# Kernel optimization log

Hardware: AMD Instinct MI355X
Metric: run time of the kernel (lower is better)

The kernel has to match this reference:

```python
import jax, jax.numpy as jnp
import numpy as np
from jax import lax

N, T, L, H, C, D, Q = 8, 8, 257, 16, 64, 1024, 256


def _ln(x, w, b, eps=1e-5):
    m = x.mean(-1, keepdims=True)
    v = ((x - m) ** 2).mean(-1, keepdims=True)
    return (x - m) * lax.rsqrt(v + eps) * w + b


def _quick_gelu(x):
    return x * jax.nn.sigmoid(1.702 * x)


def _adaptor(x, ln_w, ln_b, w1, w2):
    # LayerNorm -> Linear(d, d//8, bias=False) -> Linear(d//8, d, bias=False)
    h = _ln(x, ln_w, ln_b)
    return (h @ w1.T) @ w2.T


def setup_inputs() -> dict:
    key = jax.random.key(0)
    ks = jax.random.split(key, 16)
    f32 = jnp.float32
    inp = {
        'attrs_k': jax.random.normal(ks[0], (N, T, L, H, C), f32),
        'attrs_v': jax.random.normal(ks[1], (N, T, L, H, C), f32),
        's': jax.random.normal(ks[2], (N, Q, D), f32),
        'te': jax.random.normal(ks[3], (T, D), f32),
        'patch_mask': jax.random.normal(ks[4], (1, 1, Q, L - 1, 1), f32) * 0.1,
        'ln1_w': jnp.ones((D,), f32), 'ln1_b': jnp.zeros((D,), f32),
        'in_proj_w': jax.random.normal(ks[5], (3 * D, D), f32) * 0.02,
        'in_proj_b': jnp.zeros((3 * D,), f32),
        'out_proj_w': jax.random.normal(ks[6], (D, D), f32) * 0.02,
        'out_proj_b': jnp.zeros((D,), f32),
        'ln2_w': jnp.ones((D,), f32), 'ln2_b': jnp.zeros((D,), f32),
        'c_fc_w': jax.random.normal(ks[7], (4 * D, D), f32) * 0.02,
        'c_fc_b': jnp.zeros((4 * D,), f32),
        'c_proj_w': jax.random.normal(ks[8], (D, 4 * D), f32) * 0.02,
        'c_proj_b': jnp.zeros((D,), f32),
        'syno_ln_w': jnp.ones((D,), f32), 'syno_ln_b': jnp.zeros((D,), f32),
        'syno_l1_w': jax.random.normal(ks[9], (D // 8, D), f32) * 0.001,
        'syno_l2_w': jax.random.normal(ks[10], (D, D // 8), f32) * 0.001,
        'te_ln_w': jnp.ones((D,), f32), 'te_ln_b': jnp.zeros((D,), f32),
        'te_l1_w': jax.random.normal(ks[11], (D // 8, D), f32) * 0.001,
        'te_l2_w': jax.random.normal(ks[12], (D, D // 8), f32) * 0.001,
        'tconv_w': jax.random.normal(ks[13], (D, 1, 3), f32) * 0.001,
        'tconv_b': jnp.zeros((D,), f32),
    }
    return inp


def reference(attrs_k, attrs_v, s, te, patch_mask,
              ln1_w, ln1_b, in_proj_w, in_proj_b, out_proj_w, out_proj_b,
              ln2_w, ln2_b, c_fc_w, c_fc_b, c_proj_w, c_proj_b,
              syno_ln_w, syno_ln_b, syno_l1_w, syno_l2_w,
              te_ln_w, te_ln_b, te_l1_w, te_l2_w, tconv_w, tconv_b):
    n, q, d = s.shape
    t = te.shape[0]
    h = H
    c = d // h

    # adaptors (forward())
    _te = _adaptor(te, te_ln_w, te_ln_b, te_l1_w, te_l2_w) + te
    _s = s + _adaptor(s, syno_ln_w, syno_ln_b, syno_l1_w, syno_l2_w)
    x = _ln(_s, ln1_w, ln1_b)

    # qkv projections
    qkv = x @ in_proj_w.T + in_proj_b
    s_q, _, _ = jnp.split(qkv, 3, axis=-1)
    s_q = s_q.reshape(n, q, h, c)
    te_qkv = _te @ in_proj_w.T + in_proj_b
    _, te_k, te_v = jnp.split(te_qkv, 3, axis=-1)
    te_k = te_k.reshape(t, 1, h, c)  # broadcasts over batch and k dims
    te_v = te_v.reshape(t, 1, h, c)

    _k = attrs_k[:, :, 1:]  # drop CLS -> [n,t,K,h,c]
    _v = attrs_v[:, :, 1:]

    scale = 1.0 / jnp.sqrt(jnp.asarray(c, s_q.dtype))
    s_aff = jnp.einsum('nqhc,ntkhc->ntqkh', s_q * scale, _k + te_k) + patch_mask
    s_aff = jax.nn.softmax(s_aff, axis=-2)  # over k
    s_mix = jnp.einsum('ntqkh,ntkhc->ntqhc', s_aff, _v + te_v)

    # residual depthwise temporal conv over t: [n,t,q,h,c] -> [n*q, d, t]
    xm = s_mix.transpose(0, 2, 3, 4, 1).reshape(n * q, d, t)
    y = lax.conv_general_dilated(xm, tconv_w, window_strides=(1,), padding=[(1, 1)],
                                 feature_group_count=d,
                                 dimension_numbers=('NCH', 'OIH', 'NCH'))
    xm = (y + tconv_b[None, :, None]) + xm
    s_mix = xm.reshape(n, q, h, c, t).transpose(0, 4, 1, 2, 3)  # [n,t,q,h,c]

    s_mix = s_mix.mean(axis=1)  # mean over time -> [n,q,h,c]
    s_out = s_mix.reshape(n, q, d) @ out_proj_w.T + out_proj_b

    # residual + MLP (CLIP-style QuickGELU)
    s1 = s + s_out
    hmid = _quick_gelu(_ln(s1, ln2_w, ln2_b) @ c_fc_w.T + c_fc_b)
    s1 = s1 + (hmid @ c_proj_w.T + c_proj_b)
    return s1
```

## Files before the change

kernel.cpp:

```cpp
#include <hip/hip_runtime.h>

#define NN 8
#define TT 8
#define LL 257
#define HH 16
#define CC 64
#define DD 1024
#define QQ 256
#define NQ (NN*QQ)

typedef __attribute__((ext_vector_type(4))) float f32x4;
typedef __attribute__((ext_vector_type(4))) unsigned int u32x4;
typedef __attribute__((ext_vector_type(2))) unsigned int u32x2;

static __device__ __forceinline__ float4 ld4(const float* p) { return *(const float4*)p; }

static __device__ __forceinline__ void mfma16(f32x4& d, u32x4 a, u32x4 b) {
  asm("v_mfma_f32_16x16x32_bf16 %0, %1, %2, %0" : "+v"(d) : "v"(a), "v"(b));
}

static __device__ __forceinline__ unsigned int f2bf(float x) {
  unsigned int u = __float_as_uint(x);
  return (u + 0x7fffu + ((u >> 16) & 1u)) >> 16;
}
static __device__ __forceinline__ unsigned int pk2(float lo, float hi) {
  return f2bf(lo) | (f2bf(hi) << 16);
}
static __device__ __forceinline__ unsigned int cvtpk(float lo, float hi) {
  unsigned int r;
  asm("v_cvt_pk_bf16_f32 %0, %1, %2" : "=v"(r) : "v"(lo), "v"(hi));
  return r;
}
static __device__ __forceinline__ float bf2f(unsigned int u) {
  return __uint_as_float(u << 16);
}

typedef __attribute__((address_space(3))) unsigned char lds_t;
typedef const __attribute__((address_space(1))) unsigned char glb_t;
static __device__ __forceinline__ void gld16(const void* g, void* l) {
  __builtin_amdgcn_global_load_lds((glb_t*)g, (lds_t*)l, 16, 0, 0);
}

__global__ __launch_bounds__(256) void cvt_bf16_kernel(const float* __restrict__ in,
    unsigned short* __restrict__ out, int n4) {
  const int i = blockIdx.x * 256 + threadIdx.x;
  if (i < n4) {
    const float4 v = ld4(in + (size_t)i * 4);
    u32x2 p; p.x = pk2(v.x, v.y); p.y = pk2(v.z, v.w);
    *(u32x2*)(out + (size_t)i * 4) = p;
  }
}

__global__ __launch_bounds__(256) void ln_bf_kernel(const float* __restrict__ in,
    const float* __restrict__ w, const float* __restrict__ b, unsigned short* __restrict__ out) {
  __shared__ float red[16];
  const int tid = threadIdx.x;
  const size_t row = blockIdx.x;
  const float4 v = ((const float4*)(in + row * DD))[tid];
  float s  = v.x + v.y + v.z + v.w;
  float ss = v.x*v.x + v.y*v.y + v.z*v.z + v.w*v.w;
  #pragma unroll
  for (int off = 32; off; off >>= 1) { s += __shfl_xor(s, off); ss += __shfl_xor(ss, off); }
  if ((tid & 63) == 0) { red[tid >> 6] = s; red[8 + (tid >> 6)] = ss; }
  __syncthreads();
  s  = red[0] + red[1] + red[2] + red[3];
  ss = red[8] + red[9] + red[10] + red[11];
  const float mean = s * (1.f / DD);
  const float var  = ss * (1.f / DD) - mean * mean;
  const float inv  = rsqrtf(var + 1e-5f);
  const float4 wv = ((const float4*)w)[tid];
  const float4 bv = ((const float4*)b)[tid];
  float o0 = (v.x - mean) * inv * wv.x + bv.x;
  float o1 = (v.y - mean) * inv * wv.y + bv.y;
  float o2 = (v.z - mean) * inv * wv.z + bv.z;
  float o3 = (v.w - mean) * inv * wv.w + bv.w;
  u32x2 p; p.x = pk2(o0, o1); p.y = pk2(o2, o3);
  *(u32x2*)(out + row * DD + tid * 4) = p;
}

__global__ __launch_bounds__(256) void te_mid_kernel(
    const unsigned short* __restrict__ telnb, const float* __restrict__ l1,
    float* __restrict__ midf) {
  const int j = blockIdx.x * 4 + (threadIdx.x >> 6);
  const int l = threadIdx.x & 63;
  const float* lr = l1 + (size_t)j * DD + l * 16;
  float wv[16];
  #pragma unroll
  for (int q = 0; q < 4; ++q) {
    const float4 f = ld4(lr + q * 4);
    wv[q*4] = f.x; wv[q*4+1] = f.y; wv[q*4+2] = f.z; wv[q*4+3] = f.w;
  }
  float acc[8];
  #pragma unroll
  for (int t = 0; t < 8; ++t) {
    const unsigned short* hp = telnb + (size_t)t * DD + l * 16;
    const u32x4 h0 = *(const u32x4*)hp;
    const u32x4 h1 = *(const u32x4*)(hp + 8);
    float a = 0.f;
    #pragma unroll
    for (int e = 0; e < 4; ++e) {
      a += bf2f(h0[e] & 0xffffu) * wv[e*2]   + bf2f(h0[e] >> 16) * wv[e*2+1];
      a += bf2f(h1[e] & 0xffffu) * wv[8+e*2] + bf2f(h1[e] >> 16) * wv[8+e*2+1];
    }
    acc[t] = a;
  }
  #pragma unroll
  for (int off = 1; off < 64; off <<= 1)
    #pragma unroll
    for (int t = 0; t < 8; ++t) acc[t] += __shfl_xor(acc[t], off);
  if (l == 0) {
    #pragma unroll
    for (int t = 0; t < 8; ++t) midf[t * 128 + j] = acc[t];
  }
}

__global__ __launch_bounds__(256) void te_fin_kernel(
    const float* __restrict__ midf, const float* __restrict__ l2,
    const float* __restrict__ te, float* __restrict__ tef) {
  __shared__ float mid_s[8 * 128];
  const int tid = threadIdx.x;
  ((f32x4*)mid_s)[tid] = ((const f32x4*)midf)[tid];
  __syncthreads();
  const int d = blockIdx.x * 32 + (tid >> 3);
  const int jseg = (tid & 7) * 16;
  const float* l2r = l2 + (size_t)d * 128 + jseg;
  float wv[16];
  #pragma unroll
  for (int q = 0; q < 4; ++q) {
    const float4 f = ld4(l2r + q * 4);
    wv[q*4] = f.x; wv[q*4+1] = f.y; wv[q*4+2] = f.z; wv[q*4+3] = f.w;
  }
  float acc[8];
  #pragma unroll
  for (int t = 0; t < 8; ++t) {
    float a = 0.f;
    #pragma unroll
    for (int i = 0; i < 16; ++i) a += mid_s[t * 128 + jseg + i] * wv[i];
    acc[t] = a;
  }
  #pragma unroll
  for (int off = 1; off < 8; off <<= 1)
    #pragma unroll
    for (int t = 0; t < 8; ++t) acc[t] += __shfl_xor(acc[t], off);
  if ((tid & 7) == 0) {
    #pragma unroll
    for (int t = 0; t < 8; ++t)
      tef[(size_t)t * DD + d] = te[(size_t)t * DD + d] + acc[t];
  }
}

__global__ __launch_bounds__(256) void te_kv2_kernel(
    const float* __restrict__ tef, const float* __restrict__ W, const float* __restrict__ bias,
    float* __restrict__ tek, float* __restrict__ tev) {
  __shared__ float tes[8 * 1024];
  const int tid = threadIdx.x;
  #pragma unroll
  for (int i = 0; i < 8; ++i)
    ((f32x4*)tes)[tid + i * 256] = ((const f32x4*)tef)[tid + i * 256];
  __syncthreads();
  const int o = blockIdx.x * 32 + (tid >> 3);
  const int ks0 = (tid & 7) * 128;
  const float* wr = W + (size_t)(1024 + o) * DD + ks0;
  float acc[8] = {};
  for (int kk = 0; kk < 128; kk += 4) {
    const float4 w4 = ld4(wr + kk);
    #pragma unroll
    for (int t = 0; t < 8; ++t) {
      const float4 h4 = ld4(tes + t * 1024 + ks0 + kk);
      acc[t] += w4.x*h4.x + w4.y*h4.y + w4.z*h4.z + w4.w*h4.w;
    }
  }
  #pragma unroll
  for (int off = 1; off < 8; off <<= 1)
    #pragma unroll
    for (int t = 0; t < 8; ++t) acc[t] += __shfl_xor(acc[t], off);
  if ((tid & 7) == 0) {
    const float bv = bias[1024 + o];
    float* dst = (o < 1024) ? tek : tev;
    const int oc = o & 1023;
    #pragma unroll
    for (int t = 0; t < 8; ++t) dst[(size_t)t * DD + oc] = acc[t] + bv;
  }
}

template<int EPI, int BM>
__global__ __launch_bounds__(256, 2) void gemm_bf(
    const unsigned short* __restrict__ A, const unsigned short* __restrict__ W,
    const float* __restrict__ bias, const float* __restrict__ res,
    void* __restrict__ Cv, int M, int N, int K) {
  constexpr int FR = BM / 32;
  __shared__ unsigned short As[2][BM * 64];
  __shared__ unsigned short Bs[2][128 * 64];
  const int tid = threadIdx.x, w = tid >> 6, l = tid & 63;
  const int lc = l & 15, lg = l >> 4;
  const int m0 = blockIdx.y * BM, n0 = blockIdx.x * 128;
  const int wm = (w >> 1) * (BM / 2), wn = (w & 1) * 64;
  const int rrow = tid >> 3;
  const int sblk = (tid & 7) ^ (rrow & 7);

  f32x4 acc[FR][4] = {};

  auto stagef = [&](int kt, int b) {
    const int k0 = kt * 64 + sblk * 8;
    #pragma unroll
    for (int r = 0; r < FR; ++r)
      gld16(A + (size_t)(m0 + r * 32 + rrow) * K + k0, &As[b][r * 2048 + w * 512]);
    #pragma unroll
    for (int r = 0; r < 4; ++r)
      gld16(W + (size_t)(n0 + r * 32 + rrow) * K + k0, &Bs[b][r * 2048 + w * 512]);
  };
  auto computef = [&](int b) {
    const int bx = lc & 7;
    #pragma unroll
    for (int ks = 0; ks < 2; ++ks) {
      u32x4 af[FR], bfr[4];
      #pragma unroll
      for (int i = 0; i < FR; ++i)
        af[i] = *(const u32x4*)&As[b][(wm + i * 16 + lc) * 64 + (((ks * 4 + lg) ^ bx)) * 8];
      #pragma unroll
      for (int j = 0; j < 4; ++j)
        bfr[j] = *(const u32x4*)&Bs[b][(wn + j * 16 + lc) * 64 + (((ks * 4 + lg) ^ bx)) * 8];
      #pragma unroll
      for (int i = 0; i < FR; ++i)
        #pragma unroll
        for (int j = 0; j < 4; ++j)
          mfma16(acc[i][j], af[i], bfr[j]);
    }
  };

  const int NT = K >> 6;
  stagef(0, 0);
  asm volatile("s_waitcnt vmcnt(0)" ::: "memory");
  __builtin_amdgcn_s_barrier();
  int cur = 0;
  for (int kt = 0; kt < NT - 1; ++kt) {
    stagef(kt + 1, cur ^ 1);
    computef(cur);
    asm volatile("s_waitcnt vmcnt(0)" ::: "memory");
    __builtin_amdgcn_s_barrier();
    cur ^= 1;
  }
  computef(cur);

  float bias4[4];
  if (EPI == 1 || EPI == 2 || EPI == 3) {
    #pragma unroll
    for (int j = 0; j < 4; ++j) bias4[j] = bias[n0 + wn + j * 16 + lc];
  }
  #pragma unroll
  for (int i = 0; i < FR; ++i) {
    #pragma unroll
    for (int j = 0; j < 4; ++j) {
      const int col = n0 + wn + j * 16 + lc;
      #pragma unroll
      for (int r = 0; r < 4; ++r) {
        const int row = m0 + wm + i * 16 + lg * 4 + r;
        float x = acc[i][j][r];
        if (EPI == 0) {
          ((unsigned short*)Cv)[(size_t)row * N + col] = (unsigned short)f2bf(x);
        } else if (EPI == 1) {
          x = (x + bias4[j]) * 0.125f;
          ((unsigned short*)Cv)[(size_t)row * N + col] = (unsigned short)f2bf(x);
        } else if (EPI == 2) {
          x += bias4[j];
          x = x / (1.f + __expf(-1.702f * x));
          ((unsigned short*)Cv)[(size_t)row * N + col] = (unsigned short)f2bf(x);
        } else if (EPI == 3) {
          x += bias4[j] + res[(size_t)row * N + col];
          ((float*)Cv)[(size_t)row * N + col] = x;
        } else {
          x += res[(size_t)row * N + col];
          ((float*)Cv)[(size_t)row * N + col] = x;
        }
      }
    }
  }
}

__global__ __launch_bounds__(256, 2) void attn_mfma(
    const float* __restrict__ ak, const float* __restrict__ av,
    const unsigned short* __restrict__ qbf,
    const float* __restrict__ tek, const float* __restrict__ tev,
    const float* __restrict__ mask, unsigned short* __restrict__ smix) {
  const int h = blockIdx.x, t = blockIdx.y, n = blockIdx.z;
  const int tid = threadIdx.x, w = tid >> 6, l = tid & 63;
  const int lc = l & 15, lg = l >> 4;
  __shared__ unsigned short Ks[64][72];
  __shared__ unsigned short Vt[64][72];
  __shared__ unsigned short Pl[4][64][72];

  u32x4 qf[4][2];
  {
    const unsigned short* qb = qbf + ((size_t)(n * QQ + w * 64 + lc)) * DD + h * CC + lg * 8;
    #pragma unroll
    for (int fnq = 0; fnq < 4; ++fnq)
      #pragma unroll
      for (int ks = 0; ks < 2; ++ks)
        qf[fnq][ks] = *(const u32x4*)(qb + (size_t)fnq * 16 * DD + ks * 32);
  }
  float qte4[4];
  {
    float tkc[16];
    const float* tp = tek + (size_t)t * DD + h * CC + lg * 8;
    #pragma unroll
    for (int ks = 0; ks < 2; ++ks) {
      const float4 a = ld4(tp + ks * 32);
      const float4 b = ld4(tp + ks * 32 + 4);
      tkc[ks*8]   = a.x; tkc[ks*8+1] = a.y; tkc[ks*8+2] = a.z; tkc[ks*8+3] = a.w;
      tkc[ks*8+4] = b.x; tkc[ks*8+5] = b.y; tkc[ks*8+6] = b.z; tkc[ks*8+7] = b.w;
    }
    #pragma unroll
    for (int fnq = 0; fnq < 4; ++fnq) {
      float p = 0.f;
      #pragma unroll
      for (int ks = 0; ks < 2; ++ks)
        #pragma unroll
        for (int e = 0; e < 4; ++e) {
          const unsigned int u = qf[fnq][ks][e];
          p += bf2f(u & 0xffffu) * tkc[ks*8 + e*2];
          p += bf2f(u >> 16)     * tkc[ks*8 + e*2 + 1];
        }
      p += __shfl_xor(p, 16);
      p += __shfl_xor(p, 32);
      qte4[fnq] = p;
    }
  }

  f32x4 oacc[4][4] = {};
  float mrun[4], lrun[4];
  #pragma unroll
  for (int i = 0; i < 4; ++i) { mrun[i] = -1e30f; lrun[i] = 0.f; }

  const size_t krow0 = (((size_t)(n * TT + t) * LL + 1) * HH + h) * CC;
  const float* mbase = mask + (size_t)(w * 64) * QQ;

  for (int c0 = 0; c0 < QQ; c0 += 64) {
    __syncthreads();
    {
      const int kr = tid >> 2, cs = (tid & 3) * 16;
      const float* kp = ak + krow0 + (size_t)(c0 + kr) * (HH * CC) + cs;
      const float4 k0 = ld4(kp), k1 = ld4(kp + 4), k2 = ld4(kp + 8), k3 = ld4(kp + 12);
      u32x4 pa; pa.x = cvtpk(k0.x, k0.y); pa.y = cvtpk(k0.z, k0.w);
      pa.z = cvtpk(k1.x, k1.y); pa.w = cvtpk(k1.z, k1.w);
      u32x4 pb; pb.x = cvtpk(k2.x, k2.y); pb.y = cvtpk(k2.z, k2.w);
      pb.z = cvtpk(k3.x, k3.y); pb.w = cvtpk(k3.z, k3.w);
      *(u32x4*)&Ks[kr][cs] = pa;
      *(u32x4*)&Ks[kr][cs + 8] = pb;
    }
    {
      const int kp2 = tid & 31, ch = tid >> 5;
      const float* vr0 = av + krow0 + (size_t)(c0 + 2 * kp2) * (HH * CC) + ch * 8;
      const float* vr1 = vr0 + HH * CC;
      const float4 a0 = ld4(vr0), a1 = ld4(vr0 + 4);
      const float4 b0 = ld4(vr1), b1 = ld4(vr1 + 4);
      const float va[8] = {a0.x,a0.y,a0.z,a0.w,a1.x,a1.y,a1.z,a1.w};
      const float vb[8] = {b0.x,b0.y,b0.z,b0.w,b1.x,b1.y,b1.z,b1.w};
      #pragma unroll
      for (int i = 0; i < 8; ++i)
        *(unsigned int*)&Vt[ch * 8 + i][2 * kp2] = cvtpk(va[i], vb[i]);
    }
    __syncthreads();

    f32x4 sf[4][4] = {};
    #pragma unroll
    for (int ks = 0; ks < 2; ++ks) {
      u32x4 kf[4];
      #pragma unroll
      for (int fmk = 0; fmk < 4; ++fmk)
        kf[fmk] = *(const u32x4*)&Ks[fmk * 16 + lc][ks * 32 + lg * 8];
      #pragma unroll
      for (int fmk = 0; fmk < 4; ++fmk)
        #pragma unroll
        for (int fnq = 0; fnq < 4; ++fnq)
          mfma16(sf[fmk][fnq], kf[fmk], qf[fnq][ks]);
    }

    #pragma unroll
    for (int fnq = 0; fnq < 4; ++fnq) {
      const float* mrow = mbase + (size_t)(fnq * 16 + lc) * QQ + c0 + lg * 4;
      const float qv = qte4[fnq];
      #pragma unroll
      for (int fmk = 0; fmk < 4; ++fmk) {
        const f32x4 mk = *(const f32x4*)(mrow + fmk * 16);
        sf[fmk][fnq] += mk + qv;
      }
      float mx = -1e30f;
      #pragma unroll
      for (int fmk = 0; fmk < 4; ++fmk) {
        mx = fmaxf(mx, fmaxf(fmaxf(sf[fmk][fnq][0], sf[fmk][fnq][1]),
                             fmaxf(sf[fmk][fnq][2], sf[fmk][fnq][3])));
      }
      mx = fmaxf(mx, __shfl_xor(mx, 16));
      mx = fmaxf(mx, __shfl_xor(mx, 32));
      const float mnew = fmaxf(mrun[fnq], mx);
      const float corr = __expf(mrun[fnq] - mnew);
      mrun[fnq] = mnew;
      float ls = 0.f;
      #pragma unroll
      for (int fmk = 0; fmk < 4; ++fmk) {
        const float p0 = __expf(sf[fmk][fnq][0] - mnew);
        const float p1 = __expf(sf[fmk][fnq][1] - mnew);
        const float p2 = __expf(sf[fmk][fnq][2] - mnew);
        const float p3 = __expf(sf[fmk][fnq][3] - mnew);
        ls += (p0 + p1) + (p2 + p3);
        u32x2 pw; pw.x = cvtpk(p0, p1); pw.y = cvtpk(p2, p3);
        *(u32x2*)&Pl[w][fnq * 16 + lc][fmk * 16 + lg * 4] = pw;
      }
      ls += __shfl_xor(ls, 16);
      ls += __shfl_xor(ls, 32);
      lrun[fnq] = lrun[fnq] * corr + ls;
      #pragma unroll
      for (int fmc = 0; fmc < 4; ++fmc) oacc[fmc][fnq] *= corr;
    }

    #pragma unroll
    for (int ks = 0; ks < 2; ++ks) {
      u32x4 vf[4], pf[4];
      #pragma unroll
      for (int fmc = 0; fmc < 4; ++fmc)
        vf[fmc] = *(const u32x4*)&Vt[fmc * 16 + lc][ks * 32 + lg * 8];
      #pragma unroll
      for (int fnq = 0; fnq < 4; ++fnq)
        pf[fnq] = *(const u32x4*)&Pl[w][fnq * 16 + lc][ks * 32 + lg * 8];
      #pragma unroll
      for (int fmc = 0; fmc < 4; ++fmc)
        #pragma unroll
        for (int fnq = 0; fnq < 4; ++fnq)
          mfma16(oacc[fmc][fnq], vf[fmc], pf[fnq]);
    }
  }

  f32x4 tev4[4];
  {
    const float* tvp = tev + (size_t)t * DD + h * CC + lg * 4;
    #pragma unroll
    for (int fmc = 0; fmc < 4; ++fmc) tev4[fmc] = *(const f32x4*)(tvp + fmc * 16);
  }
  #pragma unroll
  for (int fnq = 0; fnq < 4; ++fnq) {
    const float inv = 1.f / lrun[fnq];
    const int qg = w * 64 + fnq * 16 + lc;
    unsigned short* op = smix + ((((size_t)(n * TT + t) * QQ + qg) * HH + h) * CC + lg * 4);
    #pragma unroll
    for (int fmc = 0; fmc < 4; ++fmc) {
      const f32x4 o = oacc[fmc][fnq] * inv + tev4[fmc];
      u32x2 p; p.x = cvtpk(o[0], o[1]); p.y = cvtpk(o[2], o[3]);
      *(u32x2*)(op + fmc * 16) = p;
    }
  }
}

__global__ __launch_bounds__(256) void combine_kernel(
    const unsigned short* __restrict__ smix, const float* __restrict__ cw,
    const float* __restrict__ cb, unsigned short* __restrict__ smm) {
  const int nq = blockIdx.x;
  const int d = threadIdx.x * 4;
  const int n = nq >> 8, q = nq & 255;
  const unsigned short* base = smix + ((size_t)n * TT * QQ + q) * DD + d;
  float S[4] = {0.f, 0.f, 0.f, 0.f};
  float X0[4], X7[4];
  #pragma unroll
  for (int t = 0; t < TT; ++t) {
    const u32x2 pv = *(const u32x2*)(base + (size_t)t * QQ * DD);
    const float v[4] = {bf2f(pv.x & 0xffffu), bf2f(pv.x >> 16),
                        bf2f(pv.y & 0xffffu), bf2f(pv.y >> 16)};
    if (t == 0) { X0[0]=v[0]; X0[1]=v[1]; X0[2]=v[2]; X0[3]=v[3]; }
    if (t == 7) { X7[0]=v[0]; X7[1]=v[1]; X7[2]=v[2]; X7[3]=v[3]; }
    #pragma unroll
    for (int i = 0; i < 4; ++i) S[i] += v[i];
  }
  float o[4];
  #pragma unroll
  for (int i = 0; i < 4; ++i) {
    const int chn = d + i;
    const float w0 = cw[chn*3+0], w1 = cw[chn*3+1], w2 = cw[chn*3+2];
    o[i] = ((1.f + w0 + w1 + w2) * S[i] - w0 * X7[i] - w2 * X0[i]) * 0.125f + cb[chn];
  }
  u32x2 p; p.x = pk2(o[0], o[1]); p.y = pk2(o[2], o[3]);
  *(u32x2*)(smm + (size_t)nq * DD + d) = p;
}

extern "C" void kernel_launch(void* const* d_in, const int* in_sizes, int n_in,
                              void* d_out, int out_size, void* d_ws, size_t ws_size,
                              hipStream_t stream) {
  const float* attrs_k = (const float*)d_in[0];
  const float* attrs_v = (const float*)d_in[1];
  const float* s       = (const float*)d_in[2];
  const float* te      = (const float*)d_in[3];
  const float* pmask   = (const float*)d_in[4];
  const float* ln1_w   = (const float*)d_in[5];
  const float* ln1_b   = (const float*)d_in[6];
  const float* inW     = (const float*)d_in[7];
  const float* inB     = (const float*)d_in[8];
  const float* outW    = (const float*)d_in[9];
  const float* outB    = (const float*)d_in[10];
  const float* ln2_w   = (const float*)d_in[11];
  const float* ln2_b   = (const float*)d_in[12];
  const float* fcW     = (const float*)d_in[13];
  const float* fcB     = (const float*)d_in[14];
  const float* pjW     = (const float*)d_in[15];
  const float* pjB     = (const float*)d_in[16];
  const float* sylnW   = (const float*)d_in[17];
  const float* sylnB   = (const float*)d_in[18];
  const float* syl1    = (const float*)d_in[19];
  const float* syl2    = (const float*)d_in[20];
  const float* telnW   = (const float*)d_in[21];
  const float* telnB   = (const float*)d_in[22];
  const float* tel1    = (const float*)d_in[23];
  const float* tel2    = (const float*)d_in[24];
  const float* tconvW  = (const float*)d_in[25];
  const float* tconvB  = (const float*)d_in[26];

  float* ws = (float*)d_ws;
  float*          f_te   = ws;
  float*          f_tek  = ws + 8192;
  float*          f_tev  = ws + 16384;
  unsigned short* telnb  = (unsigned short*)(ws + 24576);
  float*          midf   = ws + 28672;
  unsigned short* syl1b  = (unsigned short*)(ws + 32768);
  unsigned short* syl2b  = (unsigned short*)(ws + 98304);
  unsigned short* midb   = (unsigned short*)(ws + 163840);
  unsigned short* bufAb  = (unsigned short*)(ws + 327680);
  unsigned short* qbf    = (unsigned short*)(ws + 851968);
  unsigned short* smmb   = (unsigned short*)(ws + 1376256);
  unsigned short* wqb    = (unsigned short*)(ws + 1900544);
  unsigned short* outwb  = (unsigned short*)(ws + 2424832);
  unsigned short* fcwb   = (unsigned short*)(ws + 2949120);
  unsigned short* pjwb   = (unsigned short*)(ws + 5046272);
  float*          bufB   = ws + 7143424;
  unsigned short* smixb  = (unsigned short*)(ws + 9240576);
  float*          s1     = ws + 9240576;
  unsigned short* hmidb  = (unsigned short*)(ws + 9240576 + 2097152);
  float*          outp   = (float*)d_out;

  cvt_bf16_kernel<<<1024, 256, 0, stream>>>(inW,  wqb,   262144);
  cvt_bf16_kernel<<<1024, 256, 0, stream>>>(outW, outwb, 262144);
  cvt_bf16_kernel<<<4096, 256, 0, stream>>>(fcW,  fcwb,  1048576);
  cvt_bf16_kernel<<<4096, 256, 0, stream>>>(pjW,  pjwb,  1048576);
  cvt_bf16_kernel<<<128,  256, 0, stream>>>(syl1, syl1b, 32768);
  cvt_bf16_kernel<<<128,  256, 0, stream>>>(syl2, syl2b, 32768);

  ln_bf_kernel<<<TT, 256, 0, stream>>>(te, telnW, telnB, telnb);
  te_mid_kernel<<<32, 256, 0, stream>>>(telnb, tel1, midf);
  te_fin_kernel<<<32, 256, 0, stream>>>(midf, tel2, te, f_te);
  te_kv2_kernel<<<64, 256, 0, stream>>>(f_te, inW, inB, f_tek, f_tev);

  ln_bf_kernel<<<NQ, 256, 0, stream>>>(s, sylnW, sylnB, bufAb);
  gemm_bf<0, 64><<<dim3(1, 32), 256, 0, stream>>>(bufAb, syl1b, nullptr, nullptr, midb, NQ, 128, DD);
  gemm_bf<4, 64><<<dim3(8, 32), 256, 0, stream>>>(midb, syl2b, nullptr, s, bufB, NQ, DD, 128);
  ln_bf_kernel<<<NQ, 256, 0, stream>>>(bufB, ln1_w, ln1_b, bufAb);
  gemm_bf<1, 64><<<dim3(8, 32), 256, 0, stream>>>(bufAb, wqb, inB, nullptr, qbf, NQ, DD, DD);
  attn_mfma<<<dim3(HH, TT, NN), 256, 0, stream>>>(attrs_k, attrs_v, qbf, f_tek, f_tev, pmask, smixb);
  combine_kernel<<<NQ, 256, 0, stream>>>(smixb, tconvW, tconvB, smmb);
  gemm_bf<3, 64><<<dim3(8, 32), 256, 0, stream>>>(smmb, outwb, outB, s, s1, NQ, DD, DD);
  ln_bf_kernel<<<NQ, 256, 0, stream>>>(s1, ln2_w, ln2_b, bufAb);
  gemm_bf<2, 128><<<dim3(32, 16), 256, 0, stream>>>(bufAb, fcwb, fcB, nullptr, hmidb, NQ, 4 * DD, DD);
  gemm_bf<3, 64><<<dim3(8, 32), 256, 0, stream>>>(hmidb, pjwb, pjB, s1, outp, NQ, DD, 4 * DD);
}
```

Baseline: 275.9 us.

## Merge weight conversions, remap GEMM blocks across XCDs, raise MFMA priority in attention

Six separate fp32-to-bf16 weight conversion launches become one kernel that picks source and destination by index range, removing launch overhead. The GEMM grids become 1D with a block-ID remap that places consecutive tiles on the same XCD (8-way interleave), aiming for better L2 reuse of shared A/W tiles. The attention kernel wraps its MFMA loops in s_setprio so the matrix work gets scheduling priority over other waves. The remap assumes the block count is divisible by 8.

```diff
diff --git a/kernel.cpp b/kernel.cpp
--- a/kernel.cpp
+++ b/kernel.cpp
@@ -41,14 +41,24 @@
   __builtin_amdgcn_global_load_lds((glb_t*)g, (lds_t*)l, 16, 0, 0);
 }
 
-__global__ __launch_bounds__(256) void cvt_bf16_kernel(const float* __restrict__ in,
-    unsigned short* __restrict__ out, int n4) {
+__global__ __launch_bounds__(256) void cvt_all_kernel(
+    const float* __restrict__ inW, const float* __restrict__ outW,
+    const float* __restrict__ fcW, const float* __restrict__ pjW,
+    const float* __restrict__ syl1, const float* __restrict__ syl2,
+    unsigned short* __restrict__ wqb, unsigned short* __restrict__ outwb,
+    unsigned short* __restrict__ fcwb, unsigned short* __restrict__ pjwb,
+    unsigned short* __restrict__ syl1b, unsigned short* __restrict__ syl2b) {
   const int i = blockIdx.x * 256 + threadIdx.x;
-  if (i < n4) {
-    const float4 v = ld4(in + (size_t)i * 4);
-    u32x2 p; p.x = pk2(v.x, v.y); p.y = pk2(v.z, v.w);
-    *(u32x2*)(out + (size_t)i * 4) = p;
-  }
+  const float* src; unsigned short* dst; int off;
+  if (i < 262144)       { src = inW;  dst = wqb;   off = i; }
+  else if (i < 524288)  { src = outW; dst = outwb; off = i - 262144; }
+  else if (i < 1572864) { src = fcW;  dst = fcwb;  off = i - 524288; }
+  else if (i < 2621440) { src = pjW;  dst = pjwb;  off = i - 1572864; }
+  else if (i < 2654208) { src = syl1; dst = syl1b; off = i - 2621440; }
+  else                  { src = syl2; dst = syl2b; off = i - 2654208; }
+  const float4 v = ld4(src + (size_t)off * 4);
+  u32x2 p; p.x = pk2(v.x, v.y); p.y = pk2(v.z, v.w);
+  *(u32x2*)(dst + (size_t)off * 4) = p;
 }
 
 __global__ __launch_bounds__(256) void ln_bf_kernel(const float* __restrict__ in,
@@ -187,13 +197,16 @@
 __global__ __launch_bounds__(256, 2) void gemm_bf(
     const unsigned short* __restrict__ A, const unsigned short* __restrict__ W,
     const float* __restrict__ bias, const float* __restrict__ res,
-    void* __restrict__ Cv, int M, int N, int K) {
+    void* __restrict__ Cv, int M, int N, int K, int ny) {
   constexpr int FR = BM / 32;
   __shared__ unsigned short As[2][BM * 64];
   __shared__ unsigned short Bs[2][128 * 64];
   const int tid = threadIdx.x, w = tid >> 6, l = tid & 63;
   const int lc = l & 15, lg = l >> 4;
-  const int m0 = blockIdx.y * BM, n0 = blockIdx.x * 128;
+  const int nb = gridDim.x;
+  const int cid = (blockIdx.x & 7) * (nb >> 3) + (blockIdx.x >> 3);
+  const int bxt = cid / ny, byt = cid - bxt * ny;
+  const int m0 = byt * BM, n0 = bxt * 128;
   const int wm = (w >> 1) * (BM / 2), wn = (w & 1) * 64;
   const int rrow = tid >> 3;
   const int sblk = (tid & 7) ^ (rrow & 7);
@@ -210,16 +223,16 @@
       gld16(W + (size_t)(n0 + r * 32 + rrow) * K + k0, &Bs[b][r * 2048 + w * 512]);
   };
   auto computef = [&](int b) {
-    const int bx = lc & 7;
+    const int kx = lc & 7;
     #pragma unroll
     for (int ks = 0; ks < 2; ++ks) {
       u32x4 af[FR], bfr[4];
       #pragma unroll
       for (int i = 0; i < FR; ++i)
-        af[i] = *(const u32x4*)&As[b][(wm + i * 16 + lc) * 64 + (((ks * 4 + lg) ^ bx)) * 8];
+        af[i] = *(const u32x4*)&As[b][(wm + i * 16 + lc) * 64 + ((ks * 4 + lg) ^ kx) * 8];
       #pragma unroll
       for (int j = 0; j < 4; ++j)
-        bfr[j] = *(const u32x4*)&Bs[b][(wn + j * 16 + lc) * 64 + (((ks * 4 + lg) ^ bx)) * 8];
+        bfr[j] = *(const u32x4*)&Bs[b][(wn + j * 16 + lc) * 64 + ((ks * 4 + lg) ^ kx) * 8];
       #pragma unroll
       for (int i = 0; i < FR; ++i)
         #pragma unroll
@@ -285,6 +298,7 @@
   const int h = blockIdx.x, t = blockIdx.y, n = blockIdx.z;
   const int tid = threadIdx.x, w = tid >> 6, l = tid & 63;
   const int lc = l & 15, lg = l >> 4;
+  constexpr int HC = HH * CC;
   __shared__ unsigned short Ks[64][72];
   __shared__ unsigned short Vt[64][72];
   __shared__ unsigned short Pl[4][64][72];
@@ -338,7 +352,7 @@
     __syncthreads();
     {
       const int kr = tid >> 2, cs = (tid & 3) * 16;
-      const float* kp = ak + krow0 + (size_t)(c0 + kr) * (HH * CC) + cs;
+      const float* kp = ak + krow0 + (size_t)(c0 + kr) * HC + cs;
       const float4 k0 = ld4(kp), k1 = ld4(kp + 4), k2 = ld4(kp + 8), k3 = ld4(kp + 12);
       u32x4 pa; pa.x = cvtpk(k0.x, k0.y); pa.y = cvtpk(k0.z, k0.w);
       pa.z = cvtpk(k1.x, k1.y); pa.w = cvtpk(k1.z, k1.w);
@@ -349,8 +363,8 @@
     }
     {
       const int kp2 = tid & 31, ch = tid >> 5;
-      const float* vr0 = av + krow0 + (size_t)(c0 + 2 * kp2) * (HH * CC) + ch * 8;
-      const float* vr1 = vr0 + HH * CC;
+      const float* vr0 = av + krow0 + (size_t)(c0 + 2 * kp2) * HC + ch * 8;
+      const float* vr1 = vr0 + HC;
       const float4 a0 = ld4(vr0), a1 = ld4(vr0 + 4);
       const float4 b0 = ld4(vr1), b1 = ld4(vr1 + 4);
       const float va[8] = {a0.x,a0.y,a0.z,a0.w,a1.x,a1.y,a1.z,a1.w};
@@ -362,6 +376,7 @@
     __syncthreads();
 
     f32x4 sf[4][4] = {};
+    __builtin_amdgcn_s_setprio(1);
     #pragma unroll
     for (int ks = 0; ks < 2; ++ks) {
       u32x4 kf[4];
@@ -374,6 +389,7 @@
         for (int fnq = 0; fnq < 4; ++fnq)
           mfma16(sf[fmk][fnq], kf[fmk], qf[fnq][ks]);
     }
+    __builtin_amdgcn_s_setprio(0);
 
     #pragma unroll
     for (int fnq = 0; fnq < 4; ++fnq) {
@@ -413,6 +429,7 @@
       for (int fmc = 0; fmc < 4; ++fmc) oacc[fmc][fnq] *= corr;
     }
 
+    __builtin_amdgcn_s_setprio(1);
     #pragma unroll
     for (int ks = 0; ks < 2; ++ks) {
       u32x4 vf[4], pf[4];
@@ -428,6 +445,7 @@
         for (int fnq = 0; fnq < 4; ++fnq)
           mfma16(oacc[fmc][fnq], vf[fmc], pf[fnq]);
     }
+    __builtin_amdgcn_s_setprio(0);
   }
 
   f32x4 tev4[4];
@@ -533,12 +551,8 @@
   unsigned short* hmidb  = (unsigned short*)(ws + 9240576 + 2097152);
   float*          outp   = (float*)d_out;
 
-  cvt_bf16_kernel<<<1024, 256, 0, stream>>>(inW,  wqb,   262144);
-  cvt_bf16_kernel<<<1024, 256, 0, stream>>>(outW, outwb, 262144);
-  cvt_bf16_kernel<<<4096, 256, 0, stream>>>(fcW,  fcwb,  1048576);
-  cvt_bf16_kernel<<<4096, 256, 0, stream>>>(pjW,  pjwb,  1048576);
-  cvt_bf16_kernel<<<128,  256, 0, stream>>>(syl1, syl1b, 32768);
-  cvt_bf16_kernel<<<128,  256, 0, stream>>>(syl2, syl2b, 32768);
+  cvt_all_kernel<<<10496, 256, 0, stream>>>(inW, outW, fcW, pjW, syl1, syl2,
+                                            wqb, outwb, fcwb, pjwb, syl1b, syl2b);
 
   ln_bf_kernel<<<TT, 256, 0, stream>>>(te, telnW, telnB, telnb);
   te_mid_kernel<<<32, 256, 0, stream>>>(telnb, tel1, midf);
@@ -546,14 +560,14 @@
   te_kv2_kernel<<<64, 256, 0, stream>>>(f_te, inW, inB, f_tek, f_tev);
 
   ln_bf_kernel<<<NQ, 256, 0, stream>>>(s, sylnW, sylnB, bufAb);
-  gemm_bf<0, 64><<<dim3(1, 32), 256, 0, stream>>>(bufAb, syl1b, nullptr, nullptr, midb, NQ, 128, DD);
-  gemm_bf<4, 64><<<dim3(8, 32), 256, 0, stream>>>(midb, syl2b, nullptr, s, bufB, NQ, DD, 128);
+  gemm_bf<0, 64><<<32, 256, 0, stream>>>(bufAb, syl1b, nullptr, nullptr, midb, NQ, 128, DD, 32);
+  gemm_bf<4, 64><<<256, 256, 0, stream>>>(midb, syl2b, nullptr, s, bufB, NQ, DD, 128, 32);
   ln_bf_kernel<<<NQ, 256, 0, stream>>>(bufB, ln1_w, ln1_b, bufAb);
-  gemm_bf<1, 64><<<dim3(8, 32), 256, 0, stream>>>(bufAb, wqb, inB, nullptr, qbf, NQ, DD, DD);
+  gemm_bf<1, 64><<<256, 256, 0, stream>>>(bufAb, wqb, inB, nullptr, qbf, NQ, DD, DD, 32);
   attn_mfma<<<dim3(HH, TT, NN), 256, 0, stream>>>(attrs_k, attrs_v, qbf, f_tek, f_tev, pmask, smixb);
   combine_kernel<<<NQ, 256, 0, stream>>>(smixb, tconvW, tconvB, smmb);
-  gemm_bf<3, 64><<<dim3(8, 32), 256, 0, stream>>>(smmb, outwb, outB, s, s1, NQ, DD, DD);
+  gemm_bf<3, 64><<<256, 256, 0, stream>>>(smmb, outwb, outB, s, s1, NQ, DD, DD, 32);
   ln_bf_kernel<<<NQ, 256, 0, stream>>>(s1, ln2_w, ln2_b, bufAb);
-  gemm_bf<2, 128><<<dim3(32, 16), 256, 0, stream>>>(bufAb, fcwb, fcB, nullptr, hmidb, NQ, 4 * DD, DD);
-  gemm_bf<3, 64><<<dim3(8, 32), 256, 0, stream>>>(hmidb, pjwb, pjB, s1, outp, NQ, DD, 4 * DD);
-}
+  gemm_bf<2, 128><<<512, 256, 0, stream>>>(bufAb, fcwb, fcB, nullptr, hmidb, NQ, 4 * DD, DD, 16);
+  gemm_bf<3, 64><<<256, 256, 0, stream>>>(hmidb, pjwb, pjB, s1, outp, NQ, DD, 4 * DD, 32);
+}
```

New measurement: 260.0 us. 5.8% less time.
